# Kernel tuning notes

Hardware: AMD Instinct MI355X
Metric: run time of the kernel (lower is better)

Reference implementation:

```python
import jax, jax.numpy as jnp
import numpy as np

EPS = 1e-5
GROUPS = 8


def conv2d(x, w, b, pad):
    y = jax.lax.conv_general_dilated(
        x, w, window_strides=(1, 1), padding=[(pad, pad), (pad, pad)],
        dimension_numbers=('NCHW', 'OIHW', 'NCHW'))
    return y + b[None, :, None, None]


def setup_inputs() -> dict:
    key = jax.random.key(0)
    ks = jax.random.split(key, 8)
    b, c, h, w = 32, 256, 56, 56
    cg = c // GROUPS
    x = jax.random.normal(ks[0], (b, c, h, w), dtype=jnp.float32)
    w1 = jax.random.normal(ks[1], (cg, cg, 1, 1), dtype=jnp.float32) * 0.05
    b1 = jnp.zeros((cg,), dtype=jnp.float32)
    w3a = jax.random.normal(ks[2], (cg, cg, 3, 3), dtype=jnp.float32) * 0.05
    b3a = jnp.zeros((cg,), dtype=jnp.float32)
    w3b = jax.random.normal(ks[3], (c, c, 3, 3), dtype=jnp.float32) * 0.02
    b3b = jnp.zeros((c,), dtype=jnp.float32)
    gn_w = jnp.ones((cg,), dtype=jnp.float32)
    gn_b = jnp.zeros((cg,), dtype=jnp.float32)
    return {"x": x, "w1": w1, "b1": b1, "w3a": w3a, "b3a": b3a,
            "w3b": w3b, "b3b": b3b, "gn_w": gn_w, "gn_b": gn_b}


def reference(x, w1, b1, w3a, b3a, w3b, b3b, gn_w, gn_b):
    b, c, h, w = x.shape
    cg = c // GROUPS
    bg = b * GROUPS
    gx = x.reshape(bg, cg, h, w)

    # spatial attention on grouped channels
    x_h = gx.mean(axis=3, keepdims=True)                       # [bg,cg,h,1]
    x_w = gx.mean(axis=2, keepdims=True).transpose(0, 1, 3, 2)  # [bg,cg,w,1]
    hw = conv2d(jnp.concatenate([x_h, x_w], axis=2), w1, b1, 0)
    xh, xw = hw[:, :, :h], hw[:, :, h:]
    x0 = gx * jax.nn.sigmoid(xh) * jax.nn.sigmoid(xw.transpose(0, 1, 3, 2))

    # GroupNorm with num_groups == num_channels (per-channel over HxW)
    mu = x0.mean(axis=(2, 3), keepdims=True)
    var = x0.var(axis=(2, 3), keepdims=True)
    x1 = (x0 - mu) / jnp.sqrt(var + EPS) * gn_w[None, :, None, None] + gn_b[None, :, None, None]

    x2 = conv2d(gx, w3a, b3a, 1)

    # channel softmax-matmul attention (per group)
    x11 = jax.nn.softmax(x1.mean(axis=(2, 3)), axis=-1)[:, None, :]  # [bg,1,cg]
    x12 = x1.reshape(bg, cg, h * w)
    x21 = jax.nn.softmax(x2.mean(axis=(2, 3)), axis=-1)[:, None, :]
    x22 = x2.reshape(bg, cg, h * w)
    weights1 = (jnp.matmul(x11, x22) + jnp.matmul(x21, x12)).reshape(bg, 1, h, w)

    # BatchNorm2d(affine=False), batch statistics (training mode)
    xr = x0.reshape(b, c, h, w)
    bm = xr.mean(axis=(0, 2, 3), keepdims=True)
    bv = xr.var(axis=(0, 2, 3), keepdims=True)
    x3 = (xr - bm) / jnp.sqrt(bv + EPS)

    x4 = conv2d(x, w3b, b3b, 1)

    # spatial softmax-matmul attention over full channels
    x31 = jax.nn.softmax(x3.mean(axis=1).reshape(b, 1, h * w), axis=-1)  # [b,1,hw]
    x32 = x3.reshape(b, c, h * w).transpose(0, 2, 1)                     # [b,hw,c]
    x41 = jax.nn.softmax(x4.mean(axis=1).reshape(b, 1, h * w), axis=-1)
    x42 = x4.reshape(b, c, h * w).transpose(0, 2, 1)
    weights2 = (jnp.matmul(x31, x42) + jnp.matmul(x41, x32)).reshape(b, c, 1, 1)

    return (gx * jax.nn.sigmoid(weights1)).reshape(b, c, h, w) + x * jax.nn.sigmoid(weights2)
```

## Files before the change

kernel.cpp:

```cpp
#include <hip/hip_runtime.h>
#include <math.h>

#define B  32
#define C  256
#define HH 56
#define WW 56
#define HW 3136
#define G  8
#define CG 32
#define BG 256
#define GC 8192
#define EPSF 1e-5f

typedef __attribute__((ext_vector_type(8))) short short8;
typedef __attribute__((ext_vector_type(4))) float f32x4;

#define GLOAD16(g, l) __builtin_amdgcn_global_load_lds( \
    (const __attribute__((address_space(1))) void*)(g), \
    (__attribute__((address_space(3))) void*)(l), 16, 0, 0)

__device__ __forceinline__ float sigmoidf_(float v){ return 1.0f/(1.0f+__expf(-v)); }
__device__ __forceinline__ unsigned short f2bf(float v){
  unsigned u = __builtin_bit_cast(unsigned, v);
  u = u + 0x7FFFu + ((u>>16)&1u);
  return (unsigned short)(u>>16);
}

__global__ void k1_rowcol(const float* __restrict__ x, float* __restrict__ rowm, float* __restrict__ colm){
  int gc = blockIdx.x;
  __shared__ float t[56][57];
  const float* xp = x + (size_t)gc*HW;
  for(int idx=threadIdx.x; idx<HW; idx+=blockDim.x) t[idx/56][idx%56] = xp[idx];
  __syncthreads();
  int tid = threadIdx.x;
  if(tid < 56){
    float s=0.f;
    #pragma unroll 8
    for(int j=0;j<56;j++) s+=t[tid][j];
    rowm[gc*56+tid] = s*(1.0f/56.0f);
  } else if(tid>=64 && tid<120){
    int j=tid-64; float s=0.f;
    #pragma unroll 8
    for(int i=0;i<56;i++) s+=t[i][j];
    colm[gc*56+j] = s*(1.0f/56.0f);
  }
}

__global__ void k2_hw(const float* __restrict__ rowm, const float* __restrict__ colm,
                      const float* __restrict__ w1, const float* __restrict__ b1,
                      float* __restrict__ sh, float* __restrict__ sw){
  int bg = blockIdx.x;
  __shared__ float inb[32][112];
  __shared__ float wt[32*32];
  __shared__ float bb[32];
  for(int idx=threadIdx.x; idx<32*56; idx+=blockDim.x){
    int ic=idx/56, p=idx%56;
    inb[ic][p]    = rowm[(bg*32+ic)*56+p];
    inb[ic][56+p] = colm[(bg*32+ic)*56+p];
  }
  for(int idx=threadIdx.x; idx<1024; idx+=blockDim.x) wt[idx]=w1[idx];
  if(threadIdx.x<32) bb[threadIdx.x]=b1[threadIdx.x];
  __syncthreads();
  for(int o=threadIdx.x; o<32*112; o+=blockDim.x){
    int oc=o/112, p=o%112;
    float s=bb[oc];
    #pragma unroll
    for(int ic=0;ic<32;ic++) s += wt[oc*32+ic]*inb[ic][p];
    float sg = sigmoidf_(s);
    if(p<56) sh[(bg*32+oc)*56+p]=sg; else sw[(bg*32+oc)*56+(p-56)]=sg;
  }
}

__global__ void k2b_x11(const float* __restrict__ gnb, const float* __restrict__ b3a, float* __restrict__ x11){
  __shared__ float v[32];
  if(threadIdx.x<32) v[threadIdx.x]=gnb[threadIdx.x];
  __syncthreads();
  if(threadIdx.x==0){
    float m=-1e30f; for(int i=0;i<32;i++) m=fmaxf(m,v[i]);
    float s=0.f; for(int i=0;i<32;i++){ v[i]=__expf(v[i]-m); s+=v[i]; }
    float d=0.f;
    for(int i=0;i<32;i++){ float p=v[i]/s; x11[i]=p; d+=p*b3a[i]; }
    x11[32]=d;
  }
}

__global__ void k3_stats(const float* __restrict__ x, const float* __restrict__ sh, const float* __restrict__ sw,
                         float* __restrict__ gsum, float* __restrict__ gsq){
  int gc=blockIdx.x;
  __shared__ float ssh[56], ssw[56];
  if(threadIdx.x<56) ssh[threadIdx.x]=sh[gc*56+threadIdx.x];
  else if(threadIdx.x>=64&&threadIdx.x<120) ssw[threadIdx.x-64]=sw[gc*56+threadIdx.x-64];
  __syncthreads();
  const float* xp=x+(size_t)gc*HW;
  float s=0.f,s2=0.f;
  for(int p=threadIdx.x;p<HW;p+=blockDim.x){
    float v=xp[p]*ssh[p/56]*ssw[p%56];
    s+=v; s2+=v*v;
  }
  for(int off=32;off>0;off>>=1){ s+=__shfl_down(s,off,64); s2+=__shfl_down(s2,off,64); }
  __shared__ float rs[4], rs2[4];
  int wid=threadIdx.x>>6, lane=threadIdx.x&63;
  if(lane==0){rs[wid]=s; rs2[wid]=s2;}
  __syncthreads();
  if(threadIdx.x==0){
    gsum[gc]=rs[0]+rs[1]+rs[2]+rs[3];
    gsq[gc]=rs2[0]+rs2[1]+rs2[2]+rs2[3];
  }
}

__global__ void k4a(const float* __restrict__ gsum, const float* __restrict__ gsq,
                    float* __restrict__ mu, float* __restrict__ istd){
  int gc=blockIdx.x*256+threadIdx.x;
  float m=gsum[gc]*(1.0f/HW);
  float v=gsq[gc]*(1.0f/HW)-m*m;
  mu[gc]=m; istd[gc]=rsqrtf(v+EPSF);
}

__global__ void k4b(const float* __restrict__ gsum, const float* __restrict__ gsq,
                    float* __restrict__ bm, float* __restrict__ binv){
  int c=threadIdx.x;
  float s=0.f,s2=0.f;
  for(int b=0;b<B;b++){ s+=gsum[b*256+c]; s2+=gsq[b*256+c]; }
  float m=s*(1.0f/(B*HW));
  float v=s2*(1.0f/(B*HW))-m*m;
  bm[c]=m; binv[c]=rsqrtf(v+EPSF);
}

__global__ __launch_bounds__(128) void k5m(const unsigned short* __restrict__ xt,
    const unsigned short* __restrict__ wta, const float* __restrict__ x11,
    float* __restrict__ w1a, float* __restrict__ cs2){
  __shared__ short Bs[6*58*32];
  int bid = blockIdx.x;
  int xcd = bid & 7; int idx = bid >> 3;
  int b = xcd + 8*(idx/112); int idx2 = idx % 112;
  int g = idx2 / 14; int pt = idx2 % 14;
  int bg = b*8 + g;
  int i0 = pt*4;
  int tid = threadIdx.x;
  int lane = tid & 63, wv = tid >> 6;
  int q = lane >> 4, rl = lane & 15;
  const unsigned short* xb = xt + (size_t)b*58*58*256 + g*32;

  #pragma unroll
  for(int issue=0; issue<11; ++issue){
    int idxl = issue*128 + tid;
    if(idxl < 1392){
      int pl = idxl >> 2, ch = idxl & 3;
      int r = pl / 58, jj = pl - r*58;
      const unsigned short* src = xb + ((size_t)(i0 + r)*58 + jj)*256 + ((ch ^ ((pl>>1)&3))<<3);
      GLOAD16(src, &Bs[idxl*8]);
    }
  }
  __syncthreads();

  f32x4 acc[2][7];
  #pragma unroll
  for(int mi=0;mi<2;mi++)
    #pragma unroll
    for(int ni=0;ni<7;ni++) acc[mi][ni]=(f32x4){0.f,0.f,0.f,0.f};

  int pr[7], pj[7];
  #pragma unroll
  for(int ni=0;ni<7;ni++){
    int px = wv*112 + ni*16 + rl;
    pr[ni] = px/56; pj[ni] = px - pr[ni]*56;
  }

  for(int tap=0; tap<9; ++tap){
    int dy = tap/3, dx = tap - dy*3;
    short8 a[2], bfr[7];
    #pragma unroll
    for(int mi=0;mi<2;mi++)
      a[mi] = *(const short8*)(wta + tap*1024 + (mi*16+rl)*32 + q*8);
    #pragma unroll
    for(int ni=0;ni<7;ni++){
      int pix = (pr[ni] + dy)*58 + pj[ni] + dx;
      int cs = q ^ ((pix>>1)&3);
      bfr[ni] = *(const short8*)&Bs[pix*32 + cs*8];
    }
    #pragma unroll
    for(int mi=0;mi<2;mi++)
      #pragma unroll
      for(int ni=0;ni<7;ni++)
        acc[mi][ni] = __builtin_amdgcn_mfma_f32_16x16x32_bf16(a[mi], bfr[ni], acc[mi][ni], 0,0,0);
  }

  float x11v[2][4];
  #pragma unroll
  for(int mi=0;mi<2;mi++)
    #pragma unroll
    for(int r=0;r<4;r++) x11v[mi][r] = x11[mi*16 + q*4 + r];
  float x11b = x11[32];
  size_t pxg0 = (size_t)bg*HW + i0*56 + wv*112;
  #pragma unroll
  for(int ni=0;ni<7;ni++){
    float s=0.f;
    #pragma unroll
    for(int mi=0;mi<2;mi++)
      #pragma unroll
      for(int r=0;r<4;r++) s += x11v[mi][r]*acc[mi][ni][r];
    s += __shfl_xor(s,16,64);
    s += __shfl_xor(s,32,64);
    if(lane<16) w1a[pxg0 + ni*16 + lane] = s + x11b;
  }
  #pragma unroll
  for(int mi=0;mi<2;mi++){
    #pragma unroll
    for(int r=0;r<4;r++){
      float s=0.f;
      #pragma unroll
      for(int ni=0;ni<7;ni++) s += acc[mi][ni][r];
      s += __shfl_xor(s,1,64);
      s += __shfl_xor(s,2,64);
      s += __shfl_xor(s,4,64);
      s += __shfl_xor(s,8,64);
      if(rl==0) atomicAdd(&cs2[bg*32 + mi*16 + q*4 + r], s);
    }
  }
}

__global__ void k6(const float* __restrict__ cs2, const float* __restrict__ b3a,
                   const float* __restrict__ mu, const float* __restrict__ istd,
                   const float* __restrict__ gnw, const float* __restrict__ gnb,
                   float* __restrict__ av, float* __restrict__ cst){
  int bg=blockIdx.x; int t=threadIdx.x;
  float m = cs2[bg*32+t]*(1.0f/HW) + b3a[t];
  float mx=m;
  for(int off=16;off>0;off>>=1) mx=fmaxf(mx,__shfl_xor(mx,off,32));
  float e=__expf(m-mx);
  float s=e;
  for(int off=16;off>0;off>>=1) s+=__shfl_xor(s,off,32);
  float x21=e/s;
  int gc=bg*32+t;
  float is=istd[gc];
  av[gc]=x21*is*gnw[t];
  float cv=x21*(gnb[t]-mu[gc]*is*gnw[t]);
  for(int off=16;off>0;off>>=1) cv+=__shfl_xor(cv,off,32);
  if(t==0) cst[bg]=cv;
}

__global__ void k7(const float* __restrict__ x, const float* __restrict__ sh, const float* __restrict__ sw,
                   const float* __restrict__ w1a, const float* __restrict__ av, const float* __restrict__ cst,
                   const float* __restrict__ binv, float* __restrict__ weights1, float* __restrict__ s3pre){
  int b=blockIdx.x/56, i=blockIdx.x%56;
  int j=threadIdx.x;
  if(j>=56) return;
  float s3=0.f;
  for(int g=0;g<8;g++){
    int bg=b*8+g;
    float wsum=0.f;
    for(int cgi=0;cgi<32;cgi++){
      int gc=bg*32+cgi;
      int c=g*32+cgi;
      float x0=x[(size_t)gc*HW+i*56+j]*sh[gc*56+i]*sw[gc*56+j];
      wsum+=av[gc]*x0;
      s3+=binv[c]*x0;
    }
    weights1[(size_t)bg*HW+i*56+j]=w1a[(size_t)bg*HW+i*56+j]+wsum+cst[bg];
  }
  s3pre[(size_t)b*HW+i*56+j]=s3*(1.0f/256.0f);
}

__global__ void k_softmax_hw(const float* __restrict__ in, float* __restrict__ out, float scale){
  int b=blockIdx.x;
  const float* ip=in+(size_t)b*HW;
  float mx=-1e30f;
  for(int p=threadIdx.x;p<HW;p+=blockDim.x) mx=fmaxf(mx,ip[p]*scale);
  for(int off=32;off>0;off>>=1) mx=fmaxf(mx,__shfl_xor(mx,off,64));
  __shared__ float red[4];
  int wid=threadIdx.x>>6, lane=threadIdx.x&63;
  if(lane==0) red[wid]=mx;
  __syncthreads();
  mx=fmaxf(fmaxf(red[0],red[1]),fmaxf(red[2],red[3]));
  float s=0.f;
  for(int p=threadIdx.x;p<HW;p+=blockDim.x) s+=__expf(ip[p]*scale-mx);
  for(int off=32;off>0;off>>=1) s+=__shfl_down(s,off,64);
  __shared__ float red2[4];
  if(lane==0) red2[wid]=s;
  __syncthreads();
  s=red2[0]+red2[1]+red2[2]+red2[3];
  float inv=1.0f/s;
  for(int p=threadIdx.x;p<HW;p+=blockDim.x) out[(size_t)b*HW+p]=__expf(ip[p]*scale-mx)*inv;
}

__global__ void kxt(const float* __restrict__ x, unsigned short* __restrict__ xt){
  int bid = blockIdx.x;
  int b = bid / 196; int r2 = bid % 196; int icb = r2 / 49; int pxb = r2 % 49;
  __shared__ float t[64][65];
  int tid = threadIdx.x;
  #pragma unroll
  for(int k=0;k<16;k++){
    int e = k*256 + tid;
    int ic = e>>6, px = e&63;
    t[ic][px] = x[((size_t)(b*256 + icb*64 + ic))*HW + pxb*64 + px];
  }
  __syncthreads();
  #pragma unroll
  for(int k=0;k<16;k++){
    int e = k*256 + tid;
    int px = e>>6, ic = e&63;
    int pxg = pxb*64 + px;
    int pi = pxg/56, pj = pxg%56;
    xt[(((size_t)b*58 + pi + 1)*58 + pj + 1)*256 + icb*64 + ic] = f2bf(t[ic][px]);
  }
}

__global__ void kwt(const float* __restrict__ w3b, unsigned short* __restrict__ wt){
  int idx = blockIdx.x*256 + threadIdx.x;
  int tap = idx >> 16; int r = idx & 65535; int oc = r >> 8; int ic = r & 255;
  wt[idx] = f2bf(w3b[((size_t)oc*256 + ic)*9 + tap]);
}

__global__ void kwta(const float* __restrict__ w3a, unsigned short* __restrict__ wta){
  int idx = blockIdx.x*256 + threadIdx.x;
  if(idx < 9216){
    int tap = idx >> 10; int r = idx & 1023; int oc = r >> 5; int ic = r & 31;
    wta[idx] = f2bf(w3a[((size_t)oc*32 + ic)*9 + tap]);
  }
}

__global__ __launch_bounds__(512) void k9m(const unsigned short* __restrict__ xt,
    const unsigned short* __restrict__ wt, const float* __restrict__ x31,
    float* __restrict__ s4pre, float* __restrict__ w2a){
  __shared__ short Ab[2][128*32];
  __shared__ short Bb[2][224*32];
  int bid = blockIdx.x;
  int xcd = bid & 7; int idx = bid >> 3;
  int b = xcd + 8*(idx/28); int rr = idx % 28;
  int pt = rr >> 1; int oct = rr & 1;
  int i0 = pt*4; int ocb = oct*128;
  int tid = threadIdx.x;
  int lane = tid & 63, wv = tid >> 6;
  int wm = wv & 3, wn = wv >> 2;
  int q = lane >> 4, rl = lane & 15;
  const unsigned short* xb = xt + (size_t)b*58*58*256;

  #define STAGE_A(BUF, TAP, IC0) do{ \
    int idxl = tid; int oc_ = idxl>>2, cs_ = idxl&3; \
    const unsigned short* src = wt + (((size_t)(TAP)*256 + ocb + oc_)*256 + (IC0) + (((cs_ ^ ((oc_>>1)&3)))<<3)); \
    GLOAD16(src, &Ab[BUF][idxl*8]); }while(0)
  #define STAGE_B(BUF, TAP, IC0) do{ \
    int dy_ = (TAP)/3, dx_ = (TAP)%3; \
    { int idxl = tid; int px_ = idxl>>2, cs_ = idxl&3; int r_ = px_/56, j_ = px_ - r_*56; \
      const unsigned short* src = xb + ((size_t)((i0 + r_ + dy_)*58 + (j_ + dx_)))*256 + (IC0) + ((cs_ ^ ((px_>>1)&3))<<3); \
      GLOAD16(src, &Bb[BUF][idxl*8]); } \
    if(tid < 384){ int idxl = tid + 512; int px_ = idxl>>2, cs_ = idxl&3; int r_ = px_/56, j_ = px_ - r_*56; \
      const unsigned short* src = xb + ((size_t)((i0 + r_ + dy_)*58 + (j_ + dx_)))*256 + (IC0) + ((cs_ ^ ((px_>>1)&3))<<3); \
      GLOAD16(src, &Bb[BUF][idxl*8]); } }while(0)

  STAGE_A(0, 0, 0);
  STAGE_B(0, 0, 0);
  __syncthreads();

  f32x4 acc[2][7];
  #pragma unroll
  for(int mi=0;mi<2;mi++)
    #pragma unroll
    for(int ni=0;ni<7;ni++) acc[mi][ni] = (f32x4){0.f,0.f,0.f,0.f};

  for(int t=0; t<72; ++t){
    int cur = t & 1;
    if(t+1 < 72){
      int tn = t+1; int tap = tn >> 3; int ic0 = (tn & 7) << 5;
      STAGE_A(cur^1, tap, ic0);
      STAGE_B(cur^1, tap, ic0);
    }
    short8 a[2], bf[7];
    #pragma unroll
    for(int mi=0;mi<2;mi++){
      int row = wm*32 + mi*16 + rl;
      int cs = q ^ ((row>>1)&3);
      a[mi] = *(const short8*)&Ab[cur][row*32 + cs*8];
    }
    #pragma unroll
    for(int ni=0;ni<7;ni++){
      int px = wn*112 + ni*16 + rl;
      int cs = q ^ ((px>>1)&3);
      bf[ni] = *(const short8*)&Bb[cur][px*32 + cs*8];
    }
    #pragma unroll
    for(int mi=0;mi<2;mi++)
      #pragma unroll
      for(int ni=0;ni<7;ni++)
        acc[mi][ni] = __builtin_amdgcn_mfma_f32_16x16x32_bf16(a[mi], bf[ni], acc[mi][ni], 0,0,0);
    __syncthreads();
  }
  #undef STAGE_A
  #undef STAGE_B

  size_t pxbase = (size_t)b*HW + i0*56 + wn*112;
  #pragma unroll
  for(int ni=0;ni<7;ni++){
    float s = 0.f;
    #pragma unroll
    for(int mi=0;mi<2;mi++){
      s += acc[mi][ni][0]+acc[mi][ni][1]+acc[mi][ni][2]+acc[mi][ni][3];
    }
    s += __shfl_xor(s, 16, 64);
    s += __shfl_xor(s, 32, 64);
    if(lane < 16) atomicAdd(&s4pre[pxbase + ni*16 + lane], s);
  }
  float x31v[7];
  #pragma unroll
  for(int ni=0;ni<7;ni++) x31v[ni] = x31[pxbase + ni*16 + rl];
  #pragma unroll
  for(int mi=0;mi<2;mi++){
    #pragma unroll
    for(int r=0;r<4;r++){
      float s = 0.f;
      #pragma unroll
      for(int ni=0;ni<7;ni++) s += x31v[ni]*acc[mi][ni][r];
      s += __shfl_xor(s, 1, 64);
      s += __shfl_xor(s, 2, 64);
      s += __shfl_xor(s, 4, 64);
      s += __shfl_xor(s, 8, 64);
      if(rl == 0) atomicAdd(&w2a[b*256 + ocb + wm*32 + mi*16 + q*4 + r], s);
    }
  }
}

__global__ void k11(const float* __restrict__ x, const float* __restrict__ sh, const float* __restrict__ sw,
                    const float* __restrict__ x41, const float* __restrict__ bm, const float* __restrict__ binv,
                    const float* __restrict__ w2a, const float* __restrict__ b3b, float* __restrict__ w2){
  int gc=blockIdx.x; int b=gc/256, c=gc%256;
  __shared__ float ssh[56], ssw[56];
  if(threadIdx.x<56) ssh[threadIdx.x]=sh[gc*56+threadIdx.x];
  else if(threadIdx.x>=64&&threadIdx.x<120) ssw[threadIdx.x-64]=sw[gc*56+threadIdx.x-64];
  __syncthreads();
  const float* xp=x+(size_t)gc*HW;
  const float* wp=x41+(size_t)b*HW;
  float s=0.f;
  for(int p=threadIdx.x;p<HW;p+=blockDim.x){
    float x0=xp[p]*ssh[p/56]*ssw[p%56];
    s+=wp[p]*x0;
  }
  for(int off=32;off>0;off>>=1) s+=__shfl_down(s,off,64);
  __shared__ float red[4];
  int wid=threadIdx.x>>6, lane=threadIdx.x&63;
  if(lane==0) red[wid]=s;
  __syncthreads();
  if(threadIdx.x==0){
    float t=red[0]+red[1]+red[2]+red[3];
    w2[gc]=w2a[gc]+b3b[c]+binv[c]*t-bm[c]*binv[c];
  }
}

__global__ void k12(const float* __restrict__ x, const float* __restrict__ weights1, const float* __restrict__ w2,
                    float* __restrict__ out){
  int gc=blockIdx.x; int bg=gc/32;
  float sg2=sigmoidf_(w2[gc]);
  const float* xp=x+(size_t)gc*HW;
  const float* w1p=weights1+(size_t)bg*HW;
  float* op=out+(size_t)gc*HW;
  for(int p=threadIdx.x;p<HW;p+=blockDim.x){
    float s1=sigmoidf_(w1p[p]);
    op[p]=xp[p]*(s1+sg2);
  }
}

extern "C" void kernel_launch(void* const* d_in, const int* in_sizes, int n_in,
                              void* d_out, int out_size, void* d_ws, size_t ws_size,
                              hipStream_t stream) {
  const float* x   = (const float*)d_in[0];
  const float* w1  = (const float*)d_in[1];
  const float* b1  = (const float*)d_in[2];
  const float* w3a = (const float*)d_in[3];
  const float* b3a = (const float*)d_in[4];
  const float* w3b = (const float*)d_in[5];
  const float* b3b = (const float*)d_in[6];
  const float* gnw = (const float*)d_in[7];
  const float* gnb = (const float*)d_in[8];
  float* out=(float*)d_out;
  float* ws=(float*)d_ws;

  float* rowm=ws;
  float* colm=rowm+458752;
  float* sh  =colm+458752;
  float* sw  =sh+458752;
  float* x11 =sw+458752;
  float* gsum=x11+64;
  float* gsq =gsum+8192;
  float* mu  =gsq+8192;
  float* istd=mu+8192;
  float* bm  =istd+8192;
  float* binv=bm+256;
  float* cs2 =binv+256;
  float* w1a =cs2+8192;
  float* av  =w1a+802816;
  float* cst =av+8192;
  float* s3  =cst+256;
  float* x31 =s3+100352;
  float* s4  =x31+100352;
  float* x41 =s4+100352;
  float* w2a =x41+100352;
  float* w2  =w2a+8192;
  float* wt1 =w2+8192;
  unsigned short* xt = (unsigned short*)(wt1 + 802816);
  unsigned short* wtb = xt + (size_t)32*58*58*256;
  unsigned short* wta = wtb + 589824;

  hipMemsetAsync(xt, 0, (size_t)32*58*58*256*2, stream);
  kxt<<<32*4*49,256,0,stream>>>(x, xt);
  kwt<<<2304,256,0,stream>>>(w3b, wtb);
  kwta<<<36,256,0,stream>>>(w3a, wta);

  k1_rowcol<<<GC,256,0,stream>>>(x,rowm,colm);
  k2_hw<<<BG,128,0,stream>>>(rowm,colm,w1,b1,sh,sw);
  k2b_x11<<<1,32,0,stream>>>(gnb,b3a,x11);
  k3_stats<<<GC,256,0,stream>>>(x,sh,sw,gsum,gsq);
  k4a<<<32,256,0,stream>>>(gsum,gsq,mu,istd);
  k4b<<<1,256,0,stream>>>(gsum,gsq,bm,binv);
  hipMemsetAsync(cs2,0,8192*sizeof(float),stream);
  k5m<<<256*14,128,0,stream>>>(xt,wta,x11,w1a,cs2);
  k6<<<BG,32,0,stream>>>(cs2,b3a,mu,istd,gnw,gnb,av,cst);
  k7<<<B*56,64,0,stream>>>(x,sh,sw,w1a,av,cst,binv,wt1,s3);
  k_softmax_hw<<<B,256,0,stream>>>(s3,x31,1.0f);
  hipMemsetAsync(w2a,0,8192*sizeof(float),stream);
  hipMemsetAsync(s4,0,(size_t)HW*B*sizeof(float),stream);
  k9m<<<32*28,512,0,stream>>>(xt,wtb,x31,s4,w2a);
  k_softmax_hw<<<B,256,0,stream>>>(s4,x41,1.0f/256.0f);
  k11<<<GC,256,0,stream>>>(x,sh,sw,x41,bm,binv,w2a,b3b,w2);
  k12<<<GC,256,0,stream>>>(x,wt1,w2,out);
}
```

Measured before the change: 399.2 us.

## Fuse final reduction with output pass and zero only conv padding halo

Merges the per-channel weights2 reduction and the final output kernel into one kernel that caches the x plane in shared memory, so x is read once instead of twice. It also moves the sigmoid of weights1 into the producer kernel, so it is computed once per group instead of once per channel. The full memset of the padded bf16 input buffer is replaced by a small kernel that zeroes only the border halo. The cost is about 12.5KB of shared memory per block in the fused kernel.

```diff
diff --git a/kernel.cpp b/kernel.cpp
--- a/kernel.cpp
+++ b/kernel.cpp
@@ -241,7 +241,7 @@
 
 __global__ void k7(const float* __restrict__ x, const float* __restrict__ sh, const float* __restrict__ sw,
                    const float* __restrict__ w1a, const float* __restrict__ av, const float* __restrict__ cst,
-                   const float* __restrict__ binv, float* __restrict__ weights1, float* __restrict__ s3pre){
+                   const float* __restrict__ binv, float* __restrict__ sg1, float* __restrict__ s3pre){
   int b=blockIdx.x/56, i=blockIdx.x%56;
   int j=threadIdx.x;
   if(j>=56) return;
@@ -256,7 +256,7 @@
       wsum+=av[gc]*x0;
       s3+=binv[c]*x0;
     }
-    weights1[(size_t)bg*HW+i*56+j]=w1a[(size_t)bg*HW+i*56+j]+wsum+cst[bg];
+    sg1[(size_t)bg*HW+i*56+j]=sigmoidf_(w1a[(size_t)bg*HW+i*56+j]+wsum+cst[bg]);
   }
   s3pre[(size_t)b*HW+i*56+j]=s3*(1.0f/256.0f);
 }
@@ -303,6 +303,17 @@
     int pi = pxg/56, pj = pxg%56;
     xt[(((size_t)b*58 + pi + 1)*58 + pj + 1)*256 + icb*64 + ic] = f2bf(t[ic][px]);
   }
+}
+
+__global__ void khalo(unsigned short* __restrict__ xt){
+  int bid = blockIdx.x;
+  int b = bid/228, hp = bid%228;
+  int pi, pj;
+  if(hp<58){pi=0;pj=hp;}
+  else if(hp<116){pi=57;pj=hp-58;}
+  else if(hp<172){pi=hp-116+1;pj=0;}
+  else {pi=hp-172+1;pj=57;}
+  xt[(((size_t)b*58+pi)*58+pj)*256 + threadIdx.x] = 0;
 }
 
 __global__ void kwt(const float* __restrict__ w3b, unsigned short* __restrict__ wt){
@@ -419,42 +430,36 @@
   }
 }
 
-__global__ void k11(const float* __restrict__ x, const float* __restrict__ sh, const float* __restrict__ sw,
-                    const float* __restrict__ x41, const float* __restrict__ bm, const float* __restrict__ binv,
-                    const float* __restrict__ w2a, const float* __restrict__ b3b, float* __restrict__ w2){
-  int gc=blockIdx.x; int b=gc/256, c=gc%256;
+__global__ __launch_bounds__(256) void k11f(const float* __restrict__ x, const float* __restrict__ sh,
+    const float* __restrict__ sw, const float* __restrict__ x41, const float* __restrict__ bm,
+    const float* __restrict__ binv, const float* __restrict__ w2a, const float* __restrict__ b3b,
+    const float* __restrict__ sg1, float* __restrict__ out){
+  int gc=blockIdx.x; int b=gc>>8, c=gc&255, bg=gc>>5;
+  __shared__ float xs[HW];
   __shared__ float ssh[56], ssw[56];
-  if(threadIdx.x<56) ssh[threadIdx.x]=sh[gc*56+threadIdx.x];
-  else if(threadIdx.x>=64&&threadIdx.x<120) ssw[threadIdx.x-64]=sw[gc*56+threadIdx.x-64];
-  __syncthreads();
+  __shared__ float red[4];
+  int tid=threadIdx.x;
+  if(tid<56) ssh[tid]=sh[gc*56+tid];
+  else if(tid>=64&&tid<120) ssw[tid-64]=sw[gc*56+tid-64];
   const float* xp=x+(size_t)gc*HW;
   const float* wp=x41+(size_t)b*HW;
+  for(int p=tid;p<HW;p+=256) xs[p]=xp[p];
+  __syncthreads();
   float s=0.f;
-  for(int p=threadIdx.x;p<HW;p+=blockDim.x){
-    float x0=xp[p]*ssh[p/56]*ssw[p%56];
+  for(int p=tid;p<HW;p+=256){
+    float x0=xs[p]*ssh[p/56]*ssw[p%56];
     s+=wp[p]*x0;
   }
   for(int off=32;off>0;off>>=1) s+=__shfl_down(s,off,64);
-  __shared__ float red[4];
-  int wid=threadIdx.x>>6, lane=threadIdx.x&63;
+  int wid=tid>>6, lane=tid&63;
   if(lane==0) red[wid]=s;
   __syncthreads();
-  if(threadIdx.x==0){
-    float t=red[0]+red[1]+red[2]+red[3];
-    w2[gc]=w2a[gc]+b3b[c]+binv[c]*t-bm[c]*binv[c];
-  }
-}
-
-__global__ void k12(const float* __restrict__ x, const float* __restrict__ weights1, const float* __restrict__ w2,
-                    float* __restrict__ out){
-  int gc=blockIdx.x; int bg=gc/32;
-  float sg2=sigmoidf_(w2[gc]);
-  const float* xp=x+(size_t)gc*HW;
-  const float* w1p=weights1+(size_t)bg*HW;
+  float t=red[0]+red[1]+red[2]+red[3];
+  float sg2=sigmoidf_(w2a[gc]+b3b[c]+binv[c]*t-bm[c]*binv[c]);
+  const float* sp=sg1+(size_t)bg*HW;
   float* op=out+(size_t)gc*HW;
-  for(int p=threadIdx.x;p<HW;p+=blockDim.x){
-    float s1=sigmoidf_(w1p[p]);
-    op[p]=xp[p]*(s1+sg2);
+  for(int p=tid;p<HW;p+=256){
+    op[p]=xs[p]*(sp[p]+sg2);
   }
 }
 
@@ -494,13 +499,13 @@
   float* x41 =s4+100352;
   float* w2a =x41+100352;
   float* w2  =w2a+8192;
-  float* wt1 =w2+8192;
-  unsigned short* xt = (unsigned short*)(wt1 + 802816);
+  float* sg1 =w2+8192;
+  unsigned short* xt = (unsigned short*)(sg1 + 802816);
   unsigned short* wtb = xt + (size_t)32*58*58*256;
   unsigned short* wta = wtb + 589824;
 
-  hipMemsetAsync(xt, 0, (size_t)32*58*58*256*2, stream);
   kxt<<<32*4*49,256,0,stream>>>(x, xt);
+  khalo<<<32*228,256,0,stream>>>(xt);
   kwt<<<2304,256,0,stream>>>(w3b, wtb);
   kwta<<<36,256,0,stream>>>(w3a, wta);
 
@@ -513,12 +518,11 @@
   hipMemsetAsync(cs2,0,8192*sizeof(float),stream);
   k5m<<<256*14,128,0,stream>>>(xt,wta,x11,w1a,cs2);
   k6<<<BG,32,0,stream>>>(cs2,b3a,mu,istd,gnw,gnb,av,cst);
-  k7<<<B*56,64,0,stream>>>(x,sh,sw,w1a,av,cst,binv,wt1,s3);
+  k7<<<B*56,64,0,stream>>>(x,sh,sw,w1a,av,cst,binv,sg1,s3);
   k_softmax_hw<<<B,256,0,stream>>>(s3,x31,1.0f);
   hipMemsetAsync(w2a,0,8192*sizeof(float),stream);
   hipMemsetAsync(s4,0,(size_t)HW*B*sizeof(float),stream);
   k9m<<<32*28,512,0,stream>>>(xt,wtb,x31,s4,w2a);
   k_softmax_hw<<<B,256,0,stream>>>(s4,x41,1.0f/256.0f);
-  k11<<<GC,256,0,stream>>>(x,sh,sw,x41,bm,binv,w2a,b3b,w2);
-  k12<<<GC,256,0,stream>>>(x,wt1,w2,out);
-}
+  k11f<<<GC,256,0,stream>>>(x,sh,sw,x41,bm,binv,w2a,b3b,sg1,out);
+}
```

Result: faster. 391.1 us (-2.0%).
